# Optimization experiments

Measured on AMD Instinct MI355X. Metric: run time of the kernel, lower is better.

Reference implementation:

```python
import jax, jax.numpy as jnp
import numpy as np

ATOM_VOC = 128
APO = 128
NHEAD = 16
D_MODEL = 512
BOND_VOC = 32
CHIRAL_VOC = 4
B, L = 4, 384


def setup_inputs() -> dict:
    key = jax.random.key(0)
    ks = jax.random.split(key, 12)
    atoms = jax.random.randint(ks[0], (B, L), 0, ATOM_VOC)
    chirals = jax.random.randint(ks[1], (B, L), 0, CHIRAL_VOC)
    coordinates = jax.random.normal(ks[2], (B, L, 3), dtype=jnp.float32)
    bonds = jax.random.randint(ks[3], (B, L, L), 0, BOND_VOC)
    # embedding tables; padding_idx rows (0) zeroed to match torch padding_idx
    atype_emb = jax.random.normal(ks[4], (ATOM_VOC, D_MODEL), dtype=jnp.float32) * 0.02
    atype_emb = atype_emb.at[0].set(0.0)
    chiral_emb = jax.random.normal(ks[5], (CHIRAL_VOC, D_MODEL), dtype=jnp.float32) * 0.02
    chiral_emb = chiral_emb.at[0].set(0.0)
    apair_w_emb = jax.random.normal(ks[6], (ATOM_VOC * ATOM_VOC, APO), dtype=jnp.float32) * 0.02
    apair_b_emb = jax.random.normal(ks[7], (ATOM_VOC * ATOM_VOC, APO), dtype=jnp.float32) * 0.02
    means = jax.random.normal(ks[8], (APO,), dtype=jnp.float32) * 0.1
    stds = jnp.ones((APO,), dtype=jnp.float32) + jax.random.normal(ks[9], (APO,), dtype=jnp.float32) * 0.1
    bond_emb = jax.random.normal(ks[10], (BOND_VOC, NHEAD), dtype=jnp.float32) * 0.02
    bond_emb = bond_emb.at[0].set(0.0)
    lin_w = jax.random.normal(ks[11], (NHEAD, APO), dtype=jnp.float32) * (1.0 / np.sqrt(APO))
    lin_b = jnp.zeros((NHEAD,), dtype=jnp.float32)
    return dict(atoms=atoms, chirals=chirals, coordinates=coordinates, bonds=bonds,
                atype_emb=atype_emb, chiral_emb=chiral_emb,
                apair_w_emb=apair_w_emb, apair_b_emb=apair_b_emb,
                means=means, stds=stds, bond_emb=bond_emb, lin_w=lin_w, lin_b=lin_b)


def reference(atoms, chirals, coordinates, bonds, atype_emb, chiral_emb,
              apair_w_emb, apair_b_emb, means, stds, bond_emb, lin_w, lin_b):
    # atoms: [b,l] int; coordinates: [b,l,3]; bonds: [b,l,l] int
    atoms_emb = atype_emb[atoms] + chiral_emb[chirals]          # [b,l,d]
    atoms_emb = jnp.transpose(atoms_emb, (1, 0, 2))             # [l,b,d]
    diff = coordinates[:, None, :, :] - coordinates[:, :, None, :]  # [b,l,l,3]
    d2 = jnp.sum(diff * diff, axis=-1)
    distances = jnp.sqrt(d2 + 1e-12)                            # [b,l,l] (eps avoids nan grad on diag)
    apair_idx = atoms[:, None, :] * ATOM_VOC + atoms[:, :, None]  # [b,l,l]
    ap = apair_w_emb[apair_idx] * distances[..., None] + apair_b_emb[apair_idx]  # [b,l,l,apo]
    s = jnp.abs(stds) + 1e-5
    ap = jnp.exp(-0.5 * jnp.square((ap - means) / s)) / (np.sqrt(2 * np.pi) * s)
    ap = jnp.einsum('bijk,hk->bijh', ap, lin_w) + lin_b + bond_emb[bonds]  # [b,l,l,nhead]
    pad = (atoms == 0)[:, None, :, None]                        # mask key atoms (dim 2)
    ap = jnp.where(pad, -jnp.inf, ap)
    ap = jnp.transpose(ap, (0, 3, 1, 2))                        # [b,nhead,l,l]
    return atoms_emb, ap
```

## Files before the change

### kernel.cpp

```cpp
#include <hip/hip_runtime.h>
#include <hip/hip_fp16.h>
#include <math.h>
#include <string.h>

#define ATOM_VOC 128
#define APO      128
#define NHEAD    16
#define D_MODEL  512
#define NB       4
#define NL       384

typedef __attribute__((ext_vector_type(8))) _Float16 f16x8;
typedef __attribute__((ext_vector_type(4))) float    f32x4;
typedef __attribute__((ext_vector_type(4))) unsigned u32x4;

#define PACK_DWORDS (ATOM_VOC * ATOM_VOC * APO)
#define BFT_SHORTS  (4 * 4 * 16 * 8)

static __device__ inline unsigned short f2h(float x) {
    __half h = __float2half(x);
    unsigned short u; memcpy(&u, &h, 2); return u;
}

__global__ __launch_bounds__(128) void pack_kernel(
    const float* __restrict__ apw, const float* __restrict__ apb,
    const float* __restrict__ means, const float* __restrict__ stds,
    const float* __restrict__ lin_w,
    unsigned* __restrict__ pack, unsigned short* __restrict__ bft, int write_bft)
{
    const int t    = threadIdx.x;
    const int v    = blockIdx.x;
    const int ai   = blockIdx.y;
    const int half = t >> 6;
    const int p    = t & 63;
    const int k0   = 2 * p, k1 = 2 * p + 1;

    const float s0  = fabsf(stds[k0]) + 1e-5f;
    const float s1  = fabsf(stds[k1]) + 1e-5f;
    const float ag0 = 0.84932180028802f / s0;
    const float ag1 = 0.84932180028802f / s1;

    const size_t srcrow = ((size_t)v * ATOM_VOC + ai) * APO;
    float x0, x1;
    if (half == 0) {
        x0 = apw[srcrow + k0] * ag0;
        x1 = apw[srcrow + k1] * ag1;
    } else {
        x0 = (apb[srcrow + k0] - means[k0]) * ag0;
        x1 = (apb[srcrow + k1] - means[k1]) * ag1;
    }
    const int dst = (p >> 5) * 64 + half * 32 + (p & 31);
    pack[((size_t)ai * ATOM_VOC + v) * APO + dst] =
        ((unsigned)f2h(x1) << 16) | f2h(x0);

    if (write_bft && v == 0 && ai == 0) {
#pragma unroll
        for (int hh = 0; hh < 2; ++hh) {
            const int cid  = t + hh * 128;
            const int ks   = cid >> 6;
            const int quad = (cid >> 4) & 3;
            const int h    = cid & 15;
            const int kb   = ks * 32 + quad * 8;
            unsigned short tmp[8];
#pragma unroll
            for (int u = 0; u < 8; ++u) {
                const int kk = kb + u;
                float z = 0.3989422804014327f / (fabsf(stds[kk]) + 1e-5f);
                tmp[u] = f2h(lin_w[h * APO + kk] * z);
            }
            memcpy(&bft[(size_t)cid * 8], tmp, 16);
        }
    }
}

__global__ __launch_bounds__(256) void atoms_emb_kernel(
    const int* __restrict__ atoms, const int* __restrict__ chirals,
    const float* __restrict__ atype_emb, const float* __restrict__ chiral_emb,
    float* __restrict__ out)
{
    const int D4 = D_MODEL / 4;
    int t = blockIdx.x * 256 + threadIdx.x;
    if (t >= NL * NB * D4) return;
    int d4 = t % D4;
    int bl = t / D4;
    int b  = bl % NB;
    int l  = bl / NB;
    int a  = atoms[b * NL + l];
    int c  = chirals[b * NL + l];
    float4 va = ((const float4*)(atype_emb  + (size_t)a * D_MODEL))[d4];
    float4 vc = ((const float4*)(chiral_emb + (size_t)c * D_MODEL))[d4];
    float4 o;
    o.x = va.x + vc.x; o.y = va.y + vc.y; o.z = va.z + vc.z; o.w = va.w + vc.w;
    ((float4*)out)[t] = o;
}

__global__ __launch_bounds__(512, 8) void ap_kernel(
    const int*            __restrict__ atoms,
    const float*          __restrict__ coords,
    const int*            __restrict__ bonds,
    const unsigned*       __restrict__ pack,
    const unsigned short* __restrict__ bft,
    const float*          __restrict__ bond_emb,
    const float*          __restrict__ lin_b,
    float*                __restrict__ out)
{
    const int i    = blockIdx.x;
    const int b    = blockIdx.y;
    const int t    = threadIdx.x;
    const int lane = t & 63;
    const int wave = t >> 6;
    const int h    = lane & 15;
    const int quad = lane >> 4;

    __shared__ unsigned tbl[ATOM_VOC * 64];

    const int ai = atoms[b * NL + i];
    const unsigned* src = pack + (size_t)ai * (ATOM_VOC * APO);

    f16x8 bfrag[4];
#pragma unroll
    for (int ks = 0; ks < 4; ++ks)
        memcpy(&bfrag[ks], bft + ((size_t)((ks * 4 + quad) * 16 + h)) * 8, 16);
    const float lbh = lin_b[h];

    const float cix = coords[((size_t)b * NL + i) * 3 + 0];
    const float ciy = coords[((size_t)b * NL + i) * 3 + 1];
    const float ciz = coords[((size_t)b * NL + i) * 3 + 2];

    int     jv[3];
    __half2 jd2[3];
#pragma unroll
    for (int it = 0; it < 3; ++it) {
        const int j = it * 128 + wave * 16 + h;
        jv[it] = atoms[b * NL + j];
        const float dx = coords[((size_t)b * NL + j) * 3 + 0] - cix;
        const float dy = coords[((size_t)b * NL + j) * 3 + 1] - ciy;
        const float dz = coords[((size_t)b * NL + j) * 3 + 2] - ciz;
        jd2[it] = __half2half2(__float2half(
            sqrtf(fmaf(dx, dx, fmaf(dy, dy, dz * dz)) + 1e-12f)));
    }

    f32x4 acc[3] = {{0.f,0.f,0.f,0.f},{0.f,0.f,0.f,0.f},{0.f,0.f,0.f,0.f}};

#pragma unroll
    for (int ph = 0; ph < 2; ++ph) {
        if (ph) __syncthreads();
#pragma unroll
        for (int itx = 0; itx < 4; ++itx) {
            int c   = itx * 512 + t;
            int row = c >> 4;
            int cc  = c & 15;
            u32x4 d = ((const u32x4*)src)[row * 32 + ph * 16 + cc];
            *(u32x4*)&tbl[row * 64 + 4 * (cc ^ (row & 15))] = d;
        }
        __syncthreads();

#pragma unroll
        for (int it = 0; it < 3; ++it) {
            const int v  = jv[it];
            const int vb = v * 64;
            const int vx = v & 15;
            const __half2 d2 = jd2[it];
#pragma unroll
            for (int ks2 = 0; ks2 < 2; ++ks2) {
                const u32x4 wch = *(const u32x4*)&tbl[vb + 4 * ((ks2 * 4 + quad) ^ vx)];
                const u32x4 bch = *(const u32x4*)&tbl[vb + 4 * ((8 + ks2 * 4 + quad) ^ vx)];
                unsigned afw[4];
#pragma unroll
                for (int q = 0; q < 4; ++q) {
                    __half2 w2, b2;
                    unsigned wd = wch[q], bd = bch[q];
                    memcpy(&w2, &wd, 4); memcpy(&b2, &bd, 4);
                    __half2 u2  = __hfma2(w2, d2, b2);
                    __half2 nm2 = __hmul2(u2, __hneg2(u2));
                    __half2 g2  = h2exp2(nm2);
                    memcpy(&afw[q], &g2, 4);
                }
                f16x8 af;
                memcpy(&af, afw, 16);
                acc[it] = __builtin_amdgcn_mfma_f32_16x16x32_f16(
                    af, bfrag[ph * 2 + ks2], acc[it], 0, 0, 0);
            }
        }
    }

    const size_t bondrow = ((size_t)b * NL + i) * NL;
    float* op = out + (((size_t)(b * NHEAD + h)) * NL + i) * NL;
#pragma unroll
    for (int it = 0; it < 3; ++it) {
        const int jb = it * 128 + wave * 16 + quad * 4;
#pragma unroll
        for (int r = 0; r < 4; ++r) {
            const int bidx = bonds[bondrow + jb + r];
            const int ajr  = atoms[b * NL + jb + r];
            float vv = acc[it][r] + lbh + bond_emb[bidx * NHEAD + h];
            if (ajr == 0) vv = -1.0e30f;
            op[jb + r] = vv;
        }
    }
}

extern "C" void kernel_launch(void* const* d_in, const int* in_sizes, int n_in,
                              void* d_out, int out_size, void* d_ws, size_t ws_size,
                              hipStream_t stream)
{
    const int*   atoms      = (const int*)d_in[0];
    const int*   chirals    = (const int*)d_in[1];
    const float* coords     = (const float*)d_in[2];
    const int*   bonds      = (const int*)d_in[3];
    const float* atype_emb  = (const float*)d_in[4];
    const float* chiral_emb = (const float*)d_in[5];
    const float* apw        = (const float*)d_in[6];
    const float* apb        = (const float*)d_in[7];
    const float* means      = (const float*)d_in[8];
    const float* stds       = (const float*)d_in[9];
    const float* bond_emb   = (const float*)d_in[10];
    const float* lin_w      = (const float*)d_in[11];
    const float* lin_b      = (const float*)d_in[12];
    float* out = (float*)d_out;

    unsigned* pack = (unsigned*)d_ws;
    unsigned short* bftp = (unsigned short*)((char*)d_ws + (size_t)PACK_DWORDS * 4);

    pack_kernel<<<dim3(ATOM_VOC, ATOM_VOC), dim3(128), 0, stream>>>(
        apw, apb, means, stds, lin_w, pack, bftp, 1);

    {
        const int total = NL * NB * (D_MODEL / 4);
        atoms_emb_kernel<<<dim3((total + 255) / 256), dim3(256), 0, stream>>>(
            atoms, chirals, atype_emb, chiral_emb, out);
    }
    {
        float* out2 = out + (size_t)NL * NB * D_MODEL;
        ap_kernel<<<dim3(NL, NB), dim3(512), 0, stream>>>(
            atoms, coords, bonds, pack, bftp, bond_emb, lin_b, out2);
    }
}
```

Measured before the change: 131.4 us.

## Bucket query atoms by type so each block reuses one staged pair table

Adds a bucketing kernel that groups (batch, row) positions by atom type into chunks of up to four, written to a work list. Each ap_kernel block now loads the full 64KB packed pair table for one atom type into LDS once and processes several rows with it, instead of reloading the table in two phases for every row. This cuts global/L2 table traffic and per-row syncs. The costs are lower occupancy from the larger LDS footprint (launch bounds lowered to 4), an extra single-block launch, and possible load imbalance with empty or overflow slots.

```diff
diff --git a/kernel.cpp b/kernel.cpp
--- a/kernel.cpp
+++ b/kernel.cpp
@@ -9,13 +9,17 @@
 #define D_MODEL  512
 #define NB       4
 #define NL       384
+#define NW       1024
+#define CHUNK_G  4
 
 typedef __attribute__((ext_vector_type(8))) _Float16 f16x8;
 typedef __attribute__((ext_vector_type(4))) float    f32x4;
 typedef __attribute__((ext_vector_type(4))) unsigned u32x4;
 
 #define PACK_DWORDS (ATOM_VOC * ATOM_VOC * APO)
-#define BFT_SHORTS  (4 * 4 * 16 * 8)
+#define PACK_BYTES  ((size_t)PACK_DWORDS * 4)
+#define BFT_BYTES   4096
+#define S_BYTES     (NB * NL * 4)
 
 static __device__ inline unsigned short f2h(float x) {
     __half h = __float2half(x);
@@ -49,8 +53,7 @@
         x0 = (apb[srcrow + k0] - means[k0]) * ag0;
         x1 = (apb[srcrow + k1] - means[k1]) * ag1;
     }
-    const int dst = (p >> 5) * 64 + half * 32 + (p & 31);
-    pack[((size_t)ai * ATOM_VOC + v) * APO + dst] =
+    pack[((size_t)ai * ATOM_VOC + v) * APO + half * 64 + p] =
         ((unsigned)f2h(x1) << 16) | f2h(x0);
 
     if (write_bft && v == 0 && ai == 0) {
@@ -69,6 +72,45 @@
                 tmp[u] = f2h(lin_w[h * APO + kk] * z);
             }
             memcpy(&bft[(size_t)cid * 8], tmp, 16);
+        }
+    }
+}
+
+__global__ __launch_bounds__(512) void bucket_kernel(
+    const int* __restrict__ atoms, int* __restrict__ S, int2* __restrict__ W)
+{
+    __shared__ int cnt[ATOM_VOC], ofs[ATOM_VOC], stt[ATOM_VOC], ovf;
+    const int t = threadIdx.x;
+    if (t < ATOM_VOC) cnt[t] = 0;
+    if (t == 0) ovf = 512;
+    for (int s = t; s < NW; s += 512) W[s] = make_int2(0, 0);
+    __syncthreads();
+    for (int p = t; p < NB * NL; p += 512)
+        atomicAdd(&cnt[atoms[p]], 1);
+    __syncthreads();
+    if (t == 0) {
+        int run = 0;
+        for (int v = 0; v < ATOM_VOC; ++v) { stt[v] = run; ofs[v] = run; run += cnt[v]; }
+    }
+    __syncthreads();
+    for (int p = t; p < NB * NL; p += 512) {
+        int pos = atomicAdd(&ofs[atoms[p]], 1);
+        S[pos] = p;
+    }
+    __syncthreads();
+    if (t < 8) {
+        int n_slot = 0;
+        for (int x = 0; x < ATOM_VOC / 8; ++x) {
+            const int v = x * 8 + t;
+            int st = stt[v], n = cnt[v];
+            while (n > 0) {
+                int c = n < CHUNK_G ? n : CHUNK_G;
+                int slot;
+                if (n_slot < 64) { slot = t + 8 * n_slot; ++n_slot; }
+                else             { slot = atomicAdd(&ovf, 1); }
+                W[slot] = make_int2(st | (c << 24), v);
+                st += c; n -= c;
+            }
         }
     }
 }
@@ -94,7 +136,7 @@
     ((float4*)out)[t] = o;
 }
 
-__global__ __launch_bounds__(512, 8) void ap_kernel(
+__global__ __launch_bounds__(512, 4) void ap_kernel(
     const int*            __restrict__ atoms,
     const float*          __restrict__ coords,
     const int*            __restrict__ bonds,
@@ -102,20 +144,35 @@
     const unsigned short* __restrict__ bft,
     const float*          __restrict__ bond_emb,
     const float*          __restrict__ lin_b,
+    const int*            __restrict__ S,
+    const int2*           __restrict__ W,
     float*                __restrict__ out)
 {
-    const int i    = blockIdx.x;
-    const int b    = blockIdx.y;
+    const int2 wk   = W[blockIdx.x];
+    const int count = wk.x >> 24;
+    if (count == 0) return;
+    const int start = wk.x & 0xFFFFFF;
+    const int vai   = wk.y;
+
     const int t    = threadIdx.x;
     const int lane = t & 63;
     const int wave = t >> 6;
     const int h    = lane & 15;
     const int quad = lane >> 4;
 
-    __shared__ unsigned tbl[ATOM_VOC * 64];
-
-    const int ai = atoms[b * NL + i];
-    const unsigned* src = pack + (size_t)ai * (ATOM_VOC * APO);
+    __shared__ unsigned tbl[ATOM_VOC * APO];
+
+    const unsigned* src = pack + (size_t)vai * (ATOM_VOC * APO);
+#pragma unroll
+    for (int it = 0; it < 8; ++it) {
+        int c   = it * 512 + t;
+        int row = c >> 5;
+        int cc  = c & 31;
+        int hlf = cc >> 4;
+        int cp  = cc & 15;
+        u32x4 d = ((const u32x4*)src)[c];
+        *(u32x4*)&tbl[row * APO + hlf * 64 + 4 * (cp ^ (row & 15))] = d;
+    }
 
     f16x8 bfrag[4];
 #pragma unroll
@@ -123,48 +180,41 @@
         memcpy(&bfrag[ks], bft + ((size_t)((ks * 4 + quad) * 16 + h)) * 8, 16);
     const float lbh = lin_b[h];
 
-    const float cix = coords[((size_t)b * NL + i) * 3 + 0];
-    const float ciy = coords[((size_t)b * NL + i) * 3 + 1];
-    const float ciz = coords[((size_t)b * NL + i) * 3 + 2];
-
-    int     jv[3];
-    __half2 jd2[3];
-#pragma unroll
-    for (int it = 0; it < 3; ++it) {
-        const int j = it * 128 + wave * 16 + h;
-        jv[it] = atoms[b * NL + j];
-        const float dx = coords[((size_t)b * NL + j) * 3 + 0] - cix;
-        const float dy = coords[((size_t)b * NL + j) * 3 + 1] - ciy;
-        const float dz = coords[((size_t)b * NL + j) * 3 + 2] - ciz;
-        jd2[it] = __half2half2(__float2half(
-            sqrtf(fmaf(dx, dx, fmaf(dy, dy, dz * dz)) + 1e-12f)));
-    }
-
-    f32x4 acc[3] = {{0.f,0.f,0.f,0.f},{0.f,0.f,0.f,0.f},{0.f,0.f,0.f,0.f}};
-
-#pragma unroll
-    for (int ph = 0; ph < 2; ++ph) {
-        if (ph) __syncthreads();
-#pragma unroll
-        for (int itx = 0; itx < 4; ++itx) {
-            int c   = itx * 512 + t;
-            int row = c >> 4;
-            int cc  = c & 15;
-            u32x4 d = ((const u32x4*)src)[row * 32 + ph * 16 + cc];
-            *(u32x4*)&tbl[row * 64 + 4 * (cc ^ (row & 15))] = d;
-        }
-        __syncthreads();
-
+    __syncthreads();
+
+    for (int e = 0; e < count; ++e) {
+        const int p = S[start + e];
+        const int b = p / NL;
+        const int i = p - b * NL;
+
+        const float cix = coords[((size_t)b * NL + i) * 3 + 0];
+        const float ciy = coords[((size_t)b * NL + i) * 3 + 1];
+        const float ciz = coords[((size_t)b * NL + i) * 3 + 2];
+
+        int     jv[3];
+        __half2 jd2[3];
+#pragma unroll
+        for (int it = 0; it < 3; ++it) {
+            const int j = it * 128 + wave * 16 + h;
+            jv[it] = atoms[b * NL + j];
+            const float dx = coords[((size_t)b * NL + j) * 3 + 0] - cix;
+            const float dy = coords[((size_t)b * NL + j) * 3 + 1] - ciy;
+            const float dz = coords[((size_t)b * NL + j) * 3 + 2] - ciz;
+            jd2[it] = __half2half2(__float2half(
+                sqrtf(fmaf(dx, dx, fmaf(dy, dy, dz * dz)) + 1e-12f)));
+        }
+
+        f32x4 acc[3] = {{0.f,0.f,0.f,0.f},{0.f,0.f,0.f,0.f},{0.f,0.f,0.f,0.f}};
 #pragma unroll
         for (int it = 0; it < 3; ++it) {
             const int v  = jv[it];
-            const int vb = v * 64;
+            const int vb = v * APO;
             const int vx = v & 15;
             const __half2 d2 = jd2[it];
 #pragma unroll
-            for (int ks2 = 0; ks2 < 2; ++ks2) {
-                const u32x4 wch = *(const u32x4*)&tbl[vb + 4 * ((ks2 * 4 + quad) ^ vx)];
-                const u32x4 bch = *(const u32x4*)&tbl[vb + 4 * ((8 + ks2 * 4 + quad) ^ vx)];
+            for (int ks = 0; ks < 4; ++ks) {
+                const u32x4 wch = *(const u32x4*)&tbl[vb + 4 * ((ks * 4 + quad) ^ vx)];
+                const u32x4 bch = *(const u32x4*)&tbl[vb + 64 + 4 * ((ks * 4 + quad) ^ vx)];
                 unsigned afw[4];
 #pragma unroll
                 for (int q = 0; q < 4; ++q) {
@@ -179,23 +229,23 @@
                 f16x8 af;
                 memcpy(&af, afw, 16);
                 acc[it] = __builtin_amdgcn_mfma_f32_16x16x32_f16(
-                    af, bfrag[ph * 2 + ks2], acc[it], 0, 0, 0);
-            }
-        }
-    }
-
-    const size_t bondrow = ((size_t)b * NL + i) * NL;
-    float* op = out + (((size_t)(b * NHEAD + h)) * NL + i) * NL;
-#pragma unroll
-    for (int it = 0; it < 3; ++it) {
-        const int jb = it * 128 + wave * 16 + quad * 4;
-#pragma unroll
-        for (int r = 0; r < 4; ++r) {
-            const int bidx = bonds[bondrow + jb + r];
-            const int ajr  = atoms[b * NL + jb + r];
-            float vv = acc[it][r] + lbh + bond_emb[bidx * NHEAD + h];
-            if (ajr == 0) vv = -1.0e30f;
-            op[jb + r] = vv;
+                    af, bfrag[ks], acc[it], 0, 0, 0);
+            }
+        }
+
+        const size_t bondrow = ((size_t)b * NL + i) * NL;
+        float* op = out + (((size_t)(b * NHEAD + h)) * NL + i) * NL;
+#pragma unroll
+        for (int it = 0; it < 3; ++it) {
+            const int jb = it * 128 + wave * 16 + quad * 4;
+#pragma unroll
+            for (int r = 0; r < 4; ++r) {
+                const int bidx = bonds[bondrow + jb + r];
+                const int ajr  = atoms[b * NL + jb + r];
+                float vv = acc[it][r] + lbh + bond_emb[bidx * NHEAD + h];
+                if (ajr == 0) vv = -1.0e30f;
+                op[jb + r] = vv;
+            }
         }
     }
 }
@@ -219,11 +269,15 @@
     const float* lin_b      = (const float*)d_in[12];
     float* out = (float*)d_out;
 
-    unsigned* pack = (unsigned*)d_ws;
-    unsigned short* bftp = (unsigned short*)((char*)d_ws + (size_t)PACK_DWORDS * 4);
+    unsigned*       pack = (unsigned*)d_ws;
+    unsigned short* bftp = (unsigned short*)((char*)d_ws + PACK_BYTES);
+    int*            Sp   = (int*) ((char*)d_ws + PACK_BYTES + BFT_BYTES);
+    int2*           Wp   = (int2*)((char*)d_ws + PACK_BYTES + BFT_BYTES + S_BYTES);
 
     pack_kernel<<<dim3(ATOM_VOC, ATOM_VOC), dim3(128), 0, stream>>>(
         apw, apb, means, stds, lin_w, pack, bftp, 1);
+
+    bucket_kernel<<<dim3(1), dim3(512), 0, stream>>>(atoms, Sp, Wp);
 
     {
         const int total = NL * NB * (D_MODEL / 4);
@@ -232,7 +286,7 @@
     }
     {
         float* out2 = out + (size_t)NL * NB * D_MODEL;
-        ap_kernel<<<dim3(NL, NB), dim3(512), 0, stream>>>(
-            atoms, coords, bonds, pack, bftp, bond_emb, lin_b, out2);
-    }
-}
+        ap_kernel<<<dim3(NW), dim3(512), 0, stream>>>(
+            atoms, coords, bonds, pack, bftp, bond_emb, lin_b, Sp, Wp, out2);
+    }
+}
```

Result: slower. 153.3 us (+16.6%).
